# Optimization experiments

Hardware: AMD Instinct MI355X
Metric: run time of the kernel (lower is better)

## Reference

```python
import jax, jax.numpy as jnp
import numpy as np

D_MODEL = 1024
N_HEADS = 16
D_K = D_MODEL // N_HEADS
THETA = 10000.0


def _rope(x, token_positions):
    # x: [b, h, s, d_k]; interleaved RoPE (pairs at even/odd positions)
    half = D_K // 2
    inv_freq = 1.0 / (THETA ** (2.0 * jnp.arange(half, dtype=jnp.float32) / D_K))  # [half]
    angles = token_positions.astype(jnp.float32)[:, None] * inv_freq[None, :]      # [s, half]
    sin, cos = jnp.sin(angles), jnp.cos(angles)
    x_even = x[..., 0::2]
    x_odd = x[..., 1::2]
    out_even = cos * x_even - sin * x_odd
    out_odd = sin * x_even + cos * x_odd
    # interleave back: [..., half, 2] -> [..., d_k]
    return jnp.stack((out_even, out_odd), axis=-1).reshape(x.shape)


def setup_inputs() -> dict:
    key = jax.random.key(0)
    kx, kq, kk, kv, ko = jax.random.split(key, 5)
    b, s = 4, 2048
    std = (2.0 / (D_MODEL + D_MODEL)) ** 0.5
    return {
        "x": jax.random.normal(kx, (b, s, D_MODEL), dtype=jnp.float32),
        "Wq": jax.random.normal(kq, (D_MODEL, D_MODEL), dtype=jnp.float32) * std,
        "Wk": jax.random.normal(kk, (D_MODEL, D_MODEL), dtype=jnp.float32) * std,
        "Wv": jax.random.normal(kv, (D_MODEL, D_MODEL), dtype=jnp.float32) * std,
        "Wo": jax.random.normal(ko, (D_MODEL, D_MODEL), dtype=jnp.float32) * std,
        "token_positions": jnp.arange(s, dtype=jnp.int32),
    }


def reference(x, Wq, Wk, Wv, Wo, token_positions):
    b, s, _ = x.shape
    split = lambda t: t.reshape(b, s, N_HEADS, D_K).transpose(0, 2, 1, 3)  # b h s d
    q = split(x @ Wq.T)
    k = split(x @ Wk.T)
    v = split(x @ Wv.T)
    q = _rope(q, token_positions)
    k = _rope(k, token_positions)
    scores = jnp.einsum("bhnd,bhmd->bhnm", q, k) / jnp.sqrt(jnp.float32(D_K))
    causal = jnp.tril(jnp.ones((s, s), dtype=bool))
    scores = jnp.where(causal, scores, -jnp.inf)
    attn = jax.nn.softmax(scores, axis=-1)
    out = jnp.einsum("bhnm,bhmd->bhnd", attn, v)
    out = out.transpose(0, 2, 1, 3).reshape(b, s, D_MODEL)
    return out @ Wo.T
```

## Files before the change

### kernel.cpp

```cpp
#include <hip/hip_runtime.h>
#include <stdint.h>

typedef __attribute__((ext_vector_type(8))) __bf16 bf16x8;
typedef __attribute__((ext_vector_type(4))) float f32x4;
typedef __attribute__((ext_vector_type(16))) float f32x16;
typedef __attribute__((ext_vector_type(8))) unsigned short ushort8;

__device__ __forceinline__ unsigned short f2bf(float f){
  union { float f; unsigned int i; } v; v.f = f;
  unsigned int r = v.i + 0x7fffu + ((v.i >> 16) & 1u);
  return (unsigned short)(r >> 16);
}
__device__ __forceinline__ void gload16(const void* g, void* l){
  __builtin_amdgcn_global_load_lds((__attribute__((address_space(1))) void*)(g),
                                   (__attribute__((address_space(3))) void*)(l),
                                   16, 0, 0);
}
__device__ __forceinline__ unsigned int cvtpk(float lo, float hi){
  unsigned int r;
  asm("v_cvt_pk_bf16_f32 %0, %1, %2" : "=v"(r) : "v"(lo), "v"(hi));
  return r;
}
__device__ __forceinline__ bf16x8 ldsw(const char* tile, int row, int colb){
  return *(const bf16x8*)(tile + row*128 + (colb ^ ((row & 7) << 4)));
}

#define SEQ   2048
#define DM    1024
#define NH    16
#define DK    64
#define BATCH 4
#define MTOT  (BATCH*SEQ)
#define NX    (MTOT*DM)
#define NW    (DM*DM)

#define QSCALE 0.18033688011112f

__global__ __launch_bounds__(256) void k_tables(const int* __restrict__ pos,
                                                float* __restrict__ tab)
{
  const int idx = blockIdx.x * 256 + threadIdx.x;
  const int s = idx >> 5, i = idx & 31;
  const float inv = __expf(-0.28782313662425575f * (float)i);
  const float a = (float)pos[s] * inv;
  tab[2*idx]   = cosf(a);
  tab[2*idx+1] = sinf(a);
}

__global__ __launch_bounds__(256) void k_convert(
    const float* __restrict__ x,  const float* __restrict__ wq,
    const float* __restrict__ wk, const float* __restrict__ wv,
    const float* __restrict__ wo,
    unsigned short* __restrict__ xb, unsigned short* __restrict__ wb)
{
  const int tid = blockIdx.x * 256 + threadIdx.x;
  const long long e = (long long)tid * 8;
  const float* src; unsigned short* dst;
  if (e < NX) { src = x + e; dst = xb + e; }
  else {
    long long j = e - NX;
    int seg = (int)(j >> 20);
    long long off = j & 1048575;
    src = (seg==0?wq:seg==1?wk:seg==2?wv:wo) + off;
    dst = wb + (size_t)seg*NW + off;
  }
  const float4 a = *(const float4*)src;
  const float4 b = *(const float4*)(src + 4);
  uint4 o;
  o.x = (unsigned int)f2bf(a.x) | ((unsigned int)f2bf(a.y) << 16);
  o.y = (unsigned int)f2bf(a.z) | ((unsigned int)f2bf(a.w) << 16);
  o.z = (unsigned int)f2bf(b.x) | ((unsigned int)f2bf(b.y) << 16);
  o.w = (unsigned int)f2bf(b.z) | ((unsigned int)f2bf(b.w) << 16);
  *(uint4*)dst = o;
}

#define BK64 64
#define NT   (DM/BK64)
#define ABUF 32768
#define BSTRIDE 49152

template<int MODE>
__global__ __launch_bounds__(512, 2) void k_gemm(
    const unsigned short* __restrict__ A,
    const unsigned short* __restrict__ Wb,
    unsigned short* __restrict__ D0,
    unsigned short* __restrict__ D1,
    unsigned short* __restrict__ D2,
    float* __restrict__ Dout,
    const float* __restrict__ tab)
{
  __shared__ __attribute__((aligned(16))) char lds_[3*BSTRIDE];
  const int tid  = threadIdx.x;
  const int lane = tid & 63;
  const int w    = tid >> 6;
  const int wm = w >> 1, wn = w & 1;

  const int bid = blockIdx.x;
  const int tq  = bid >> 3;
  const int m0  = ((bid & 7)*4 + (tq & 3)) * 256;
  const int r   = tq >> 2;
  const int n0  = (MODE == 0 ? (r & 7) : r) * 128;
  const int z   = (MODE == 0) ? (r >> 3) : 0;

  const unsigned short* W = Wb + (size_t)z * NW;
  unsigned short* Dh = (MODE == 0) ? ((z == 0) ? D0 : (z == 1) ? D1 : D2) : nullptr;
  const bool vtr = (MODE == 0) && (z == 2);

  f32x4 acc[4][4];
  #pragma unroll
  for (int i = 0; i < 4; ++i)
    #pragma unroll
    for (int j = 0; j < 4; ++j)
      acc[i][j] = (f32x4)0.0f;

  auto stA = [&](int buf, int t, int l){
    const int k0 = t * BK64;
    const int id = l*512 + tid;
    const int row = id >> 3, c = id & 7;
    gload16(A + (size_t)(m0 + row)*DM + k0 + ((c ^ (row & 7)) << 3),
            lds_ + buf*BSTRIDE + id*16);
  };
  auto stB = [&](int buf, int t, int l){
    const int k0 = t * BK64;
    const int id = l*512 + tid;
    const int row = id >> 3, c = id & 7;
    gload16(W + (size_t)(n0 + row)*DM + k0 + ((c ^ (row & 7)) << 3),
            lds_ + buf*BSTRIDE + ABUF + id*16);
  };
  auto ldA = [&](const char* Ab_, int i, int kk){
    const int row = wm*64 + i*16 + (lane & 15);
    const int c = (kk*4 + (lane >> 4)) ^ (row & 7);
    return *(const bf16x8*)(Ab_ + row*128 + (c << 4));
  };
  auto ldB = [&](const char* Bb_, int j, int kk){
    const int row = wn*64 + j*16 + (lane & 15);
    const int c = (kk*4 + (lane >> 4)) ^ (row & 7);
    return *(const bf16x8*)(Bb_ + row*128 + (c << 4));
  };

  #pragma unroll
  for (int l = 0; l < 4; ++l) stA(0, 0, l);
  stB(0, 0, 0); stB(0, 0, 1);
  #pragma unroll
  for (int l = 0; l < 4; ++l) stA(1, 1, l);
  stB(1, 1, 0); stB(1, 1, 1);
  asm volatile("s_waitcnt vmcnt(6)" ::: "memory");
  __builtin_amdgcn_s_barrier();

  int rb = 0, sb = 2;
  for (int t = 0; t < NT; ++t){
    const char* Ab_ = lds_ + rb*BSTRIDE;
    const char* Bb_ = Ab_ + ABUF;
    const bool st = (t + 2 < NT);
    bf16x8 aF0, aF1, bF[4];

    aF0 = ldA(Ab_, 0, 0); aF1 = ldA(Ab_, 1, 0);
    bF[0] = ldB(Bb_, 0, 0); bF[1] = ldB(Bb_, 1, 0);
    bF[2] = ldB(Bb_, 2, 0); bF[3] = ldB(Bb_, 3, 0);
    if (st){ stA(sb, t+2, 0); stA(sb, t+2, 1); }
    __builtin_amdgcn_s_barrier();
    asm volatile("s_waitcnt lgkmcnt(0)" ::: "memory");
    __builtin_amdgcn_s_setprio(1);
    #pragma unroll
    for (int j = 0; j < 4; ++j){
      acc[0][j] = __builtin_amdgcn_mfma_f32_16x16x32_bf16(aF0, bF[j], acc[0][j], 0, 0, 0);
      acc[1][j] = __builtin_amdgcn_mfma_f32_16x16x32_bf16(aF1, bF[j], acc[1][j], 0, 0, 0);
    }
    __builtin_amdgcn_s_setprio(0);
    __builtin_amdgcn_s_barrier();

    aF0 = ldA(Ab_, 2, 0); aF1 = ldA(Ab_, 3, 0);
    if (st){ stA(sb, t+2, 2); stA(sb, t+2, 3); }
    __builtin_amdgcn_s_barrier();
    asm volatile("s_waitcnt lgkmcnt(0)" ::: "memory");
    __builtin_amdgcn_s_setprio(1);
    #pragma unroll
    for (int j = 0; j < 4; ++j){
      acc[2][j] = __builtin_amdgcn_mfma_f32_16x16x32_bf16(aF0, bF[j], acc[2][j], 0, 0, 0);
      acc[3][j] = __builtin_amdgcn_mfma_f32_16x16x32_bf16(aF1, bF[j], acc[3][j], 0, 0, 0);
    }
    __builtin_amdgcn_s_setprio(0);
    __builtin_amdgcn_s_barrier();

    aF0 = ldA(Ab_, 0, 1); aF1 = ldA(Ab_, 1, 1);
    bF[0] = ldB(Bb_, 0, 1); bF[1] = ldB(Bb_, 1, 1);
    bF[2] = ldB(Bb_, 2, 1); bF[3] = ldB(Bb_, 3, 1);
    if (st){ stB(sb, t+2, 0); stB(sb, t+2, 1); }
    __builtin_amdgcn_s_barrier();
    asm volatile("s_waitcnt lgkmcnt(0)" ::: "memory");
    __builtin_amdgcn_s_setprio(1);
    #pragma unroll
    for (int j = 0; j < 4; ++j){
      acc[0][j] = __builtin_amdgcn_mfma_f32_16x16x32_bf16(aF0, bF[j], acc[0][j], 0, 0, 0);
      acc[1][j] = __builtin_amdgcn_mfma_f32_16x16x32_bf16(aF1, bF[j], acc[1][j], 0, 0, 0);
    }
    __builtin_amdgcn_s_setprio(0);
    __builtin_amdgcn_s_barrier();

    aF0 = ldA(Ab_, 2, 1); aF1 = ldA(Ab_, 3, 1);
    __builtin_amdgcn_s_barrier();
    asm volatile("s_waitcnt lgkmcnt(0)" ::: "memory");
    __builtin_amdgcn_s_setprio(1);
    #pragma unroll
    for (int j = 0; j < 4; ++j){
      acc[2][j] = __builtin_amdgcn_mfma_f32_16x16x32_bf16(aF0, bF[j], acc[2][j], 0, 0, 0);
      acc[3][j] = __builtin_amdgcn_mfma_f32_16x16x32_bf16(aF1, bF[j], acc[3][j], 0, 0, 0);
    }
    __builtin_amdgcn_s_setprio(0);
    if (t < NT-2)       asm volatile("s_waitcnt vmcnt(6)" ::: "memory");
    else if (t == NT-2) asm volatile("s_waitcnt vmcnt(0)" ::: "memory");
    if (t < NT-1) __builtin_amdgcn_s_barrier();

    rb = (rb == 2) ? 0 : rb + 1;
    sb = (sb == 2) ? 0 : sb + 1;
  }

  __syncthreads();

  if (MODE == 0 && vtr){
    #pragma unroll
    for (int i = 0; i < 4; ++i)
      #pragma unroll
      for (int j = 0; j < 4; ++j)
        #pragma unroll
        for (int rr = 0; rr < 4; ++rr){
          const int m = m0 + wm*64 + i*16 + ((lane >> 4) << 2) + rr;
          const int n = n0 + wn*64 + j*16 + (lane & 15);
          const int b = m >> 11, sp = m & 2047, hh = n >> 6, d = n & 63;
          *(__bf16*)&Dh[(((size_t)(b*NH + hh))*DK + d)*SEQ + sp] = (__bf16)acc[i][j][rr];
        }
  } else {
    float* T = (float*)lds_;
    #pragma unroll
    for (int i = 0; i < 4; ++i)
      #pragma unroll
      for (int j = 0; j < 4; ++j){
        const int n = wn*64 + j*16 + (lane & 15);
        #pragma unroll
        for (int rr = 0; rr < 4; ++rr){
          const int m = wm*64 + i*16 + ((lane >> 4) << 2) + rr;
          T[m*128 + (n ^ ((m & 7) << 2))] = acc[i][j][rr];
        }
      }
    __syncthreads();
    const float scale = (MODE == 0 && z == 0) ? QSCALE : 1.0f;
    #pragma unroll
    for (int k = 0; k < 8; ++k){
      const int cid = k*512 + tid;
      const int d8   = cid & 7;
      const int sp_l = (cid >> 3) & 255;
      const int h    = cid >> 11;
      const int nb   = h*64 + d8*8;
      const int sw   = (sp_l & 7) << 2;
      const f32x4 c0 = *(const f32x4*)&T[sp_l*128 + (nb ^ sw)];
      const f32x4 c1 = *(const f32x4*)&T[sp_l*128 + ((nb + 4) ^ sw)];
      if (MODE == 1){
        float* dst = Dout + (size_t)(m0 + sp_l)*DM + n0 + nb;
        *(f32x4*)dst = c0;
        *(f32x4*)(dst + 4) = c1;
      } else {
        const int mg = m0 + sp_l;
        const int bidx = mg >> 11, sp = mg & 2047;
        const float4 t01 = *(const float4*)&tab[(size_t)sp*64 + d8*8];
        const float4 t23 = *(const float4*)&tab[(size_t)sp*64 + d8*8 + 4];
        const unsigned int u0 = cvtpk((t01.x*c0[0] - t01.y*c0[1])*scale,
                                      (t01.y*c0[0] + t01.x*c0[1])*scale);
        const unsigned int u1 = cvtpk((t01.z*c0[2] - t01.w*c0[3])*scale,
                                      (t01.w*c0[2] + t01.z*c0[3])*scale);
        const unsigned int u2 = cvtpk((t23.x*c1[0] - t23.y*c1[1])*scale,
                                      (t23.y*c1[0] + t23.x*c1[1])*scale);
        const unsigned int u3 = cvtpk((t23.z*c1[2] - t23.w*c1[3])*scale,
                                      (t23.w*c1[2] + t23.z*c1[3])*scale);
        const int hh = (n0 >> 6) + h;
        uint4 ov; ov.x = u0; ov.y = u1; ov.z = u2; ov.w = u3;
        *(uint4*)(Dh + ((size_t)((bidx*NH + hh)*SEQ + sp))*DK + d8*8) = ov;
      }
    }
  }
}

__global__ __launch_bounds__(512, 4) void k_attn(const unsigned short* __restrict__ Qh,
                                                 const unsigned short* __restrict__ Kh,
                                                 const unsigned short* __restrict__ Vt,
                                                 unsigned short* __restrict__ Ab)
{
  __shared__ uint4 ldsu[4096];
  char* base = (char*)ldsu;
  const int tid  = threadIdx.x;
  const int lane = tid & 63;
  const int w    = tid >> 6;
  const int ww   = w & 3;
  const int g    = w >> 2;
  const int tl   = tid & 255;
  const int l31  = lane & 31;
  const int hl   = lane >> 5;
  char* gb = base + g*32768;

  const int jj = blockIdx.x, bh = blockIdx.y;
  const unsigned short* Qb = Qh + (size_t)bh*(SEQ*DK);
  const unsigned short* Kb = Kh + (size_t)bh*(SEQ*DK);
  const unsigned short* Vb = Vt + (size_t)bh*(SEQ*DK);
  const int b = bh >> 4, hd = bh & 15;

  for (int pass = 0; pass < 2; ++pass){
    const int qt = pass ? jj : 15 - jj;
    const int q0 = qt * 128;
    const int qbase = q0 + ww*32;

    bf16x8 qf[4];
    #pragma unroll
    for (int t = 0; t < 4; ++t)
      qf[t] = *(const bf16x8*)(Qb + (size_t)(qbase + l31)*DK + t*16 + hl*8);

    f32x16 acc0 = (f32x16)0.0f, acc1 = (f32x16)0.0f;
    float lsum = 0.0f;

    const int nk = qt + 1;
    const int tbase = g * nk;
    const int wqmax = qbase + 31;

    auto stage = [&](int buf, int ktile){
      const int k0s = ktile * 64;
      char* Kd = gb + buf*16384;
      char* Vd = Kd + 8192;
      #pragma unroll
      for (int cc = 0; cc < 2; ++cc){
        const int f = cc*256 + tl;
        const int r = f >> 3, slot = f & 7;
        const int sw = ((slot ^ (r & 7)) << 3);
        gload16(Kb + (size_t)(k0s + r)*DK + sw, Kd + (cc*256 + ww*64)*16);
        gload16(Vb + (size_t)r*SEQ + k0s + sw, Vd + (cc*256 + ww*64)*16);
      }
    };

    if (pass) __syncthreads();
    stage(0, tbase);
    __syncthreads();
    int cur = 0;

    for (int kt = 0; kt < nk; ++kt){
      const int k0 = (tbase + kt) * 64;
      if (kt + 1 < nk) stage(cur ^ 1, tbase + kt + 1);
      if (k0 <= wqmax){
        const char* Ks = gb + cur*16384;
        const char* Vs = Ks + 8192;

        f32x16 sv0 = (f32x16)0.0f, sv1 = (f32x16)0.0f;
        __builtin_amdgcn_s_setprio(1);
        #pragma unroll
        for (int t = 0; t < 4; ++t){
          const int colb = t*32 + hl*16;
          const bf16x8 a0 = ldsw(Ks, l31, colb);
          const bf16x8 a1 = ldsw(Ks, 32 + l31, colb);
          sv0 = __builtin_amdgcn_mfma_f32_32x32x16_bf16(a0, qf[t], sv0, 0, 0, 0);
          sv1 = __builtin_amdgcn_mfma_f32_32x32x16_bf16(a1, qf[t], sv1, 0, 0, 0);
        }
        __builtin_amdgcn_s_setprio(0);

        if (k0 + 63 > qbase){
          const int q = qbase + l31;
          #pragma unroll
          for (int j = 0; j < 16; ++j){
            const int kv = k0 + (j&3) + 8*(j>>2) + 4*hl;
            if (kv > q)      sv0[j] = -1e30f;
            if (kv + 32 > q) sv1[j] = -1e30f;
          }
        }

        #pragma unroll
        for (int j = 0; j < 16; ++j){
          sv0[j] = exp2f(sv0[j]);
          sv1[j] = exp2f(sv1[j]);
        }
        float ts[8];
        #pragma unroll
        for (int j = 0; j < 8; ++j)
          ts[j] = (sv0[j] + sv0[j+8]) + (sv1[j] + sv1[j+8]);
        #pragma unroll
        for (int off = 4; off; off >>= 1)
          #pragma unroll
          for (int j = 0; j < off; ++j)
            ts[j] += ts[j+off];
        lsum += ts[0] + __shfl_xor(ts[0], 32, 64);

        __builtin_amdgcn_s_setprio(1);
        #pragma unroll
        for (int t = 0; t < 4; ++t){
          f32x16& s = (t < 2) ? sv0 : sv1;
          const int b0v = (t & 1) * 8;
          const unsigned int A0 = cvtpk(s[b0v+0], s[b0v+1]);
          const unsigned int A1 = cvtpk(s[b0v+2], s[b0v+3]);
          const unsigned int B0 = cvtpk(s[b0v+4], s[b0v+5]);
          const unsigned int B1 = cvtpk(s[b0v+6], s[b0v+7]);
          const unsigned int s0 = hl ? A0 : B0;
          const unsigned int s1 = hl ? A1 : B1;
          const unsigned int r0 = (unsigned int)__shfl_xor((int)s0, 32, 64);
          const unsigned int r1 = (unsigned int)__shfl_xor((int)s1, 32, 64);
          union { unsigned int u[4]; bf16x8 v; } f;
          f.u[0] = hl ? r0 : A0; f.u[1] = hl ? r1 : A1;
          f.u[2] = hl ? B0 : r0; f.u[3] = hl ? B1 : r1;
          const int colb = t*32 + hl*16;
          const bf16x8 v0 = ldsw(Vs, l31, colb);
          const bf16x8 v1 = ldsw(Vs, 32 + l31, colb);
          acc0 = __builtin_amdgcn_mfma_f32_32x32x16_bf16(v0, f.v, acc0, 0, 0, 0);
          acc1 = __builtin_amdgcn_mfma_f32_32x32x16_bf16(v1, f.v, acc1, 0, 0, 0);
        }
        __builtin_amdgcn_s_setprio(0);
      }
      __syncthreads();
      cur ^= 1;
    }

    if (g == 1){
      char* cw = base + ww*9216 + lane*144;
      #pragma unroll
      for (int q4 = 0; q4 < 4; ++q4){
        *(f32x4*)(cw + q4*16)      = (f32x4){acc0[4*q4], acc0[4*q4+1], acc0[4*q4+2], acc0[4*q4+3]};
        *(f32x4*)(cw + 64 + q4*16) = (f32x4){acc1[4*q4], acc1[4*q4+1], acc1[4*q4+2], acc1[4*q4+3]};
      }
      *(float*)(cw + 128) = lsum;
    }
    __syncthreads();
    if (g == 0){
      const char* cr = base + ww*9216 + lane*144;
      const float l1 = *(const float*)(cr + 128);
      const float linv = 1.0f / (lsum + l1);
      unsigned short* orow = Ab + ((size_t)(b*SEQ + qbase + l31))*DM + hd*DK;
      #pragma unroll
      for (int mt = 0; mt < 2; ++mt){
        #pragma unroll
        for (int g4 = 0; g4 < 4; ++g4){
          const f32x16& a = mt ? acc1 : acc0;
          const f32x4 o = *(const f32x4*)(cr + mt*64 + g4*16);
          const unsigned int u0 = cvtpk((a[4*g4+0] + o[0])*linv, (a[4*g4+1] + o[1])*linv);
          const unsigned int u1 = cvtpk((a[4*g4+2] + o[2])*linv, (a[4*g4+3] + o[3])*linv);
          *(unsigned long long*)(orow + mt*32 + g4*8 + hl*4) =
              (unsigned long long)u0 | ((unsigned long long)u1 << 32);
        }
      }
    }
  }
}

extern "C" void kernel_launch(void* const* d_in, const int* in_sizes, int n_in,
                              void* d_out, int out_size, void* d_ws, size_t ws_size,
                              hipStream_t stream)
{
  (void)in_sizes; (void)n_in; (void)out_size;
  const float* x  = (const float*)d_in[0];
  const float* wq = (const float*)d_in[1];
  const float* wk = (const float*)d_in[2];
  const float* wv = (const float*)d_in[3];
  const float* wo = (const float*)d_in[4];
  const int* pos  = (const int*)d_in[5];
  float* out = (float*)d_out;

  if (ws_size < 92800000u) return;
  char* ws = (char*)d_ws;
  unsigned short* xb = (unsigned short*)(ws);
  unsigned short* wb = (unsigned short*)(ws + 16777216);
  unsigned short* Qh = (unsigned short*)(ws + 25165824);
  unsigned short* Kh = (unsigned short*)(ws + 41943040);
  unsigned short* Vt = (unsigned short*)(ws + 75497472);
  float* tab         = (float*)(ws + 92274688);

  k_tables  <<<256, 256, 0, stream>>>(pos, tab);
  k_convert <<<6144, 256, 0, stream>>>(x, wq, wk, wv, wo, xb, wb);
  k_gemm<0> <<<768, 512, 0, stream>>>(xb, wb, Qh, Kh, Vt, nullptr, tab);
  k_attn    <<<dim3(8, 64), 512, 0, stream>>>(Qh, Kh, Vt, xb);
  k_gemm<1> <<<256, 512, 0, stream>>>(xb, wb + 3*NW, nullptr, nullptr,
                                      nullptr, out, nullptr);
}
```

Measured before the change: 176.8 us.

## Stage V-transpose epilogue through LDS with packed stores; use raw v_exp_f32

```diff
diff --git a/kernel.cpp b/kernel.cpp
--- a/kernel.cpp
+++ b/kernel.cpp
@@ -20,6 +20,9 @@
   unsigned int r;
   asm("v_cvt_pk_bf16_f32 %0, %1, %2" : "=v"(r) : "v"(lo), "v"(hi));
   return r;
+}
+__device__ __forceinline__ float fexp2(float x){
+  float r; asm("v_exp_f32 %0, %1" : "=v"(r) : "v"(x)); return r;
 }
 __device__ __forceinline__ bf16x8 ldsw(const char* tile, int row, int colb){
   return *(const bf16x8*)(tile + row*128 + (colb ^ ((row & 7) << 4)));
@@ -217,19 +220,7 @@
 
   __syncthreads();
 
-  if (MODE == 0 && vtr){
-    #pragma unroll
-    for (int i = 0; i < 4; ++i)
-      #pragma unroll
-      for (int j = 0; j < 4; ++j)
-        #pragma unroll
-        for (int rr = 0; rr < 4; ++rr){
-          const int m = m0 + wm*64 + i*16 + ((lane >> 4) << 2) + rr;
-          const int n = n0 + wn*64 + j*16 + (lane & 15);
-          const int b = m >> 11, sp = m & 2047, hh = n >> 6, d = n & 63;
-          *(__bf16*)&Dh[(((size_t)(b*NH + hh))*DK + d)*SEQ + sp] = (__bf16)acc[i][j][rr];
-        }
-  } else {
+  {
     float* T = (float*)lds_;
     #pragma unroll
     for (int i = 0; i < 4; ++i)
@@ -242,7 +233,29 @@
           T[m*128 + (n ^ ((m & 7) << 2))] = acc[i][j][rr];
         }
       }
-    __syncthreads();
+  }
+  __syncthreads();
+  const float* T = (const float*)lds_;
+
+  if (MODE == 0 && vtr){
+    const int nl = tid >> 2;
+    const int sblk = tid & 3;
+    const int d = nl & 63, hh = (n0 >> 6) + (nl >> 6);
+    const int bidx = m0 >> 11;
+    unsigned short* vrow = Dh + (((size_t)(bidx*NH + hh))*DK + d)*SEQ + (m0 & 2047);
+    #pragma unroll
+    for (int c = 0; c < 8; ++c){
+      const int s0 = sblk*8 + c*32;
+      float v[8];
+      #pragma unroll
+      for (int j2 = 0; j2 < 8; ++j2)
+        v[j2] = T[(s0 + j2)*128 + (nl ^ (((s0 + j2) & 7) << 2))];
+      uint4 ov;
+      ov.x = cvtpk(v[0], v[1]); ov.y = cvtpk(v[2], v[3]);
+      ov.z = cvtpk(v[4], v[5]); ov.w = cvtpk(v[6], v[7]);
+      *(uint4*)(vrow + s0) = ov;
+    }
+  } else {
     const float scale = (MODE == 0 && z == 0) ? QSCALE : 1.0f;
     #pragma unroll
     for (int k = 0; k < 8; ++k){
@@ -369,8 +382,8 @@
 
         #pragma unroll
         for (int j = 0; j < 16; ++j){
-          sv0[j] = exp2f(sv0[j]);
-          sv1[j] = exp2f(sv1[j]);
+          sv0[j] = fexp2(sv0[j]);
+          sv1[j] = fexp2(sv1[j]);
         }
         float ts[8];
         #pragma unroll
```

After: 164.6 us. 6.9% less time.
